# Kernel tuning notes

Hardware: AMD Instinct MI355X
Metric: run time of the kernel (lower is better)

The kernel has to match this reference:

```python
import jax, jax.numpy as jnp
import numpy as np

N = 100000          # nodes
E = 800000          # edges
H = 32              # hidden_features
L = 4               # num_layers
HS = 32             # hidden_edge_scores
EPS_BN = 1e-5
EPS_AGG = 1e-6


def _bn(x, g, b):
    # training-mode batch norm over the node/edge (batch) axis
    mu = jnp.mean(x, axis=0)
    var = jnp.var(x, axis=0)
    return (x - mu) * jax.lax.rsqrt(var + EPS_BN) * g + b


def setup_inputs() -> dict:
    key = jax.random.key(0)
    ks = jax.random.split(key, 24)
    rn = lambda k, s, sc=0.1: jax.random.normal(k, s, dtype=jnp.float32) * sc
    return {
        "x": rn(ks[0], (N, 1), 1.0),
        "e": rn(ks[1], (E, 1), 1.0),
        "edge_index": jax.random.randint(ks[2], (2, E), 0, N),
        # input projections
        "pe_w": rn(ks[3], (1, H)), "pe_b": rn(ks[4], (H,)),
        "ed_w": rn(ks[5], (1, H)), "ed_b": rn(ks[6], (H,)),
        # per-layer GatedGCN weights, stacked over layers
        "A_w": rn(ks[7], (L, H, H)), "A_b": rn(ks[8], (L, H)),
        "B_w": rn(ks[9], (L, H, H)), "B_b": rn(ks[10], (L, H)),
        "C_w": rn(ks[11], (L, H, H)), "C_b": rn(ks[12], (L, H)),
        "U_w": rn(ks[13], (L, H, H)), "U_b": rn(ks[14], (L, H)),
        "V_w": rn(ks[15], (L, H, H)), "V_b": rn(ks[16], (L, H)),
        # batch-norm affine params
        "bn_h_g": jnp.ones((L, H), jnp.float32), "bn_h_b": jnp.zeros((L, H), jnp.float32),
        "bn_e_g": jnp.ones((L, H), jnp.float32), "bn_e_b": jnp.zeros((L, H), jnp.float32),
        # score predictor: concat(src_h, dst_h, e) -> HS -> 1
        "W1_w": rn(ks[17], (3 * H, HS)), "W1_b": rn(ks[18], (HS,)),
        "W2_w": rn(ks[19], (HS, 1)), "W2_b": rn(ks[20], (1,)),
    }


def reference(x, e, edge_index, pe_w, pe_b, ed_w, ed_b,
              A_w, A_b, B_w, B_b, C_w, C_b, U_w, U_b, V_w, V_b,
              bn_h_g, bn_h_b, bn_e_g, bn_e_b, W1_w, W1_b, W2_w, W2_b):
    src, dst = edge_index[0], edge_index[1]
    h = x @ pe_w + pe_b          # [N, H]
    e = e @ ed_w + ed_b          # [E, H]
    n = h.shape[0]
    for l in range(L):
        Ah = h @ A_w[l] + A_b[l]
        Bh = h @ B_w[l] + B_b[l]
        Ce = e @ C_w[l] + C_b[l]
        Uh = h @ U_w[l] + U_b[l]
        Vh = h @ V_w[l] + V_b[l]
        # edge update: gather node features to edges
        e_new = Ah[dst] + Bh[src] + Ce               # [E, H]
        sigma = jax.nn.sigmoid(e_new)                # edge gates
        # gated mean aggregation: scatter-add to dst nodes
        num = jax.ops.segment_sum(sigma * Vh[src], dst, num_segments=n)
        den = jax.ops.segment_sum(sigma, dst, num_segments=n)
        h_new = Uh + num / (den + EPS_AGG)           # [N, H]
        # BN -> ReLU -> residual
        h = h + jax.nn.relu(_bn(h_new, bn_h_g[l], bn_h_b[l]))
        e = e + jax.nn.relu(_bn(e_new, bn_e_g[l], bn_e_b[l]))
    # score predictor over edges
    z = jnp.concatenate([h[src], h[dst], e], axis=1)  # [E, 3H]
    scores = jax.nn.relu(z @ W1_w + W1_b) @ W2_w + W2_b  # [E, 1]
    return scores
```

## Files before the change

### kernel.cpp

```cpp
#include <hip/hip_runtime.h>
#include <hip/hip_bf16.h>
#include <hip/hip_fp16.h>

#define NLAYERS 4
#define GRID_STRIDE 2048

typedef _Float16 half8_t __attribute__((ext_vector_type(8)));
typedef float float4_t __attribute__((ext_vector_type(4)));
typedef float float8_t __attribute__((ext_vector_type(8)));

__device__ __forceinline__ int permcol(int pos) { return (pos >> 1) | ((pos & 1) << 4); }

__device__ __forceinline__ void unp4(uint2 r, float* f)
{
    float2 a = __half22float2(*(__half2*)&r.x);
    float2 b = __half22float2(*(__half2*)&r.y);
    f[0] = a.x; f[1] = a.y; f[2] = b.x; f[3] = b.y;
}

__device__ __forceinline__ uint2 pk4(float f0, float f1, float f2, float f3)
{
    __half2 a = __floats2half2_rn(f0, f1), b = __floats2half2_rn(f2, f3);
    uint2 r;
    r.x = *(unsigned*)&a; r.y = *(unsigned*)&b;
    return r;
}

__global__ void zero_ints(int* __restrict__ p, int n)
{
    int i = blockIdx.x * 256 + threadIdx.x;
    if (i < n) p[i] = 0;
}

__global__ void hist_kernel(const int* __restrict__ dsts, int* __restrict__ counts, int E)
{
    int i = blockIdx.x * 256 + threadIdx.x;
    if (i < E) atomicAdd(&counts[dsts[i]], 1);
}

__global__ __launch_bounds__(256) void scan1(const int* __restrict__ counts,
                                             int* __restrict__ offsets,
                                             int* __restrict__ blocksums, int N)
{
    __shared__ int sdata[256];
    int t = threadIdx.x;
    int bbase = blockIdx.x * 1024;
    int v[4]; int s = 0;
#pragma unroll
    for (int q = 0; q < 4; q++) {
        int idx = bbase + t * 4 + q;
        v[q] = (idx < N) ? counts[idx] : 0;
        s += v[q];
    }
    sdata[t] = s;
    __syncthreads();
    for (int off = 1; off < 256; off <<= 1) {
        int x = (t >= off) ? sdata[t - off] : 0;
        __syncthreads();
        sdata[t] += x;
        __syncthreads();
    }
    int excl = sdata[t] - s;
    int run = excl;
#pragma unroll
    for (int q = 0; q < 4; q++) {
        int idx = bbase + t * 4 + q;
        if (idx < N) offsets[idx] = run;
        run += v[q];
    }
    if (t == 255) blocksums[blockIdx.x] = sdata[255];
}

__global__ void scan2(int* __restrict__ blocksums, int nb)
{
    if (threadIdx.x == 0 && blockIdx.x == 0) {
        int run = 0;
        for (int b = 0; b < nb; b++) { int t = blocksums[b]; blocksums[b] = run; run += t; }
    }
}

__global__ void scan3(int* __restrict__ offsets, const int* __restrict__ blocksums,
                      int* __restrict__ cursor, int N)
{
    int i = blockIdx.x * 256 + threadIdx.x;
    if (i < N) {
        int v = offsets[i] + blocksums[i >> 10];
        offsets[i] = v;
        cursor[i] = v;
    }
}

__global__ void scatter_perm(const int* __restrict__ dsts, int* __restrict__ cursor,
                             int* __restrict__ perm, int E, int N)
{
    int g = blockIdx.x & 7;
    int lo = (int)((long long)N * g >> 3);
    int hi = (int)((long long)N * (g + 1) >> 3);
    int nbg = gridDim.x >> 3;
    int bg = blockIdx.x >> 3;
    for (int i = bg * 256 + threadIdx.x; i < E; i += nbg * 256) {
        int d = dsts[i];
        if (d >= lo && d < hi) {
            int slot = atomicAdd(&cursor[d], 1);
            perm[slot] = i;
        }
    }
}

__global__ void gather_sd(const int* __restrict__ perm, const int* __restrict__ srcs,
                          const int* __restrict__ dsts, int* __restrict__ srcp,
                          int* __restrict__ dstp, int E)
{
    int i = blockIdx.x * 256 + threadIdx.x;
    if (i < E) {
        int e = perm[i];
        srcp[i] = srcs[e];
        dstp[i] = dsts[e];
    }
}

__global__ void init_proj4(const float* __restrict__ in, const float* __restrict__ w,
                           const float* __restrict__ b, float4* __restrict__ out, size_t n4)
{
    size_t i = (size_t)blockIdx.x * 256 + threadIdx.x;
    if (i < n4) {
        int j4 = (int)(i & 7) * 4;
        float xv = in[i >> 3];
        int c0 = permcol(j4), c1 = permcol(j4 + 1), c2 = permcol(j4 + 2), c3 = permcol(j4 + 3);
        out[i] = make_float4(fmaf(xv, w[c0], b[c0]), fmaf(xv, w[c1], b[c1]),
                             fmaf(xv, w[c2], b[c2]), fmaf(xv, w[c3], b[c3]));
    }
}

__global__ void init_ep16(const float* __restrict__ e_in, const int* __restrict__ perm,
                          const float* __restrict__ w, const float* __restrict__ b,
                          __half2* __restrict__ out, size_t n4)
{
    size_t i = (size_t)blockIdx.x * 256 + threadIdx.x;
    if (i < n4) {
        int row = (int)(i >> 3);
        float xv = e_in[perm[row]];
        int j4 = (int)(i & 7) * 4;
        int c0 = permcol(j4), c1 = permcol(j4 + 1), c2 = permcol(j4 + 2), c3 = permcol(j4 + 3);
        out[i * 2]     = __floats2half2_rn(fmaf(xv, w[c0], b[c0]), fmaf(xv, w[c1], b[c1]));
        out[i * 2 + 1] = __floats2half2_rn(fmaf(xv, w[c2], b[c2]), fmaf(xv, w[c3], b[c3]));
    }
}

template <int FUSE>
__global__ __launch_bounds__(256) void node_gemm(
    float* __restrict__ h, const float* __restrict__ hnew_in,
    const float* __restrict__ sc_h, const float* __restrict__ sh_h,
    const float* __restrict__ Aw, const float* __restrict__ Ab,
    const float* __restrict__ Bw, const float* __restrict__ Bb,
    const float* __restrict__ Uw, const float* __restrict__ Ub,
    const float* __restrict__ Vw, const float* __restrict__ Vb,
    __half* __restrict__ Ahh, __half* __restrict__ Bhh,
    float* __restrict__ Uhh, __half* __restrict__ Vhh, int N)
{
    int tid = threadIdx.x;
    int lane = tid & 63;
    int m = lane & 15, q = lane >> 4;
    half8_t bA0, bA1, bB0, bB1, bU0, bU1, bV0, bV1;
    float scq[8], shq[8];
#pragma unroll
    for (int i = 0; i < 8; i++) {
        int k = q * 8 + i;
        int kr = permcol(k);
        bA0[i] = (_Float16)Aw[kr * 32 + m];  bA1[i] = (_Float16)Aw[kr * 32 + m + 16];
        bB0[i] = (_Float16)Bw[kr * 32 + m];  bB1[i] = (_Float16)Bw[kr * 32 + m + 16];
        bU0[i] = (_Float16)Uw[kr * 32 + m];  bU1[i] = (_Float16)Uw[kr * 32 + m + 16];
        bV0[i] = (_Float16)Vw[kr * 32 + m];  bV1[i] = (_Float16)Vw[kr * 32 + m + 16];
        if (FUSE) { scq[i] = sc_h[k]; shq[i] = sh_h[k]; }
    }
    float ab0 = Ab[m], ab1 = Ab[m + 16];
    float bb0 = Bb[m], bb1 = Bb[m + 16];
    float ub0 = Ub[m], ub1 = Ub[m + 16];
    float vb0 = Vb[m], vb1 = Vb[m + 16];

    int ntile = (N + 15) >> 4;
    int wid = blockIdx.x * 4 + (tid >> 6);
    int nwave = gridDim.x * 4;
    for (int t = wid; t < ntile; t += nwave) {
        int base = t << 4;
        int arow = base + m;
        bool valid = arow < N;
        if (!valid) arow = N - 1;
        float8_t hv = *(const float8_t*)(h + (size_t)arow * 32 + q * 8);
        if (FUSE) {
            float8_t pv = *(const float8_t*)(hnew_in + (size_t)arow * 32 + q * 8);
#pragma unroll
            for (int i = 0; i < 8; i++)
                hv[i] += fmaxf(fmaf(pv[i], scq[i], shq[i]), 0.f);
            if (valid) *(float8_t*)(h + (size_t)arow * 32 + q * 8) = hv;
        }
        half8_t a;
#pragma unroll
        for (int i = 0; i < 8; i++) a[i] = (_Float16)hv[i];
        float4_t aA0 = __builtin_amdgcn_mfma_f32_16x16x32_f16(a, bA0, (float4_t){0,0,0,0}, 0, 0, 0);
        float4_t aA1 = __builtin_amdgcn_mfma_f32_16x16x32_f16(a, bA1, (float4_t){0,0,0,0}, 0, 0, 0);
        float4_t aB0 = __builtin_amdgcn_mfma_f32_16x16x32_f16(a, bB0, (float4_t){0,0,0,0}, 0, 0, 0);
        float4_t aB1 = __builtin_amdgcn_mfma_f32_16x16x32_f16(a, bB1, (float4_t){0,0,0,0}, 0, 0, 0);
        float4_t aU0 = __builtin_amdgcn_mfma_f32_16x16x32_f16(a, bU0, (float4_t){0,0,0,0}, 0, 0, 0);
        float4_t aU1 = __builtin_amdgcn_mfma_f32_16x16x32_f16(a, bU1, (float4_t){0,0,0,0}, 0, 0, 0);
        float4_t aV0 = __builtin_amdgcn_mfma_f32_16x16x32_f16(a, bV0, (float4_t){0,0,0,0}, 0, 0, 0);
        float4_t aV1 = __builtin_amdgcn_mfma_f32_16x16x32_f16(a, bV1, (float4_t){0,0,0,0}, 0, 0, 0);
#pragma unroll
        for (int reg = 0; reg < 4; reg++) {
            int node = base + q * 4 + reg;
            if (node < N) {
                size_t o = (size_t)node * 32;
                *(__half2*)(Ahh + o + 2 * m) = __floats2half2_rn(aA0[reg] + ab0, aA1[reg] + ab1);
                *(__half2*)(Bhh + o + 2 * m) = __floats2half2_rn(aB0[reg] + bb0, aB1[reg] + bb1);
                *(__half2*)(Vhh + o + 2 * m) = __floats2half2_rn(aV0[reg] + vb0, aV1[reg] + vb1);
                *(float2*)(Uhh + o + 2 * m)  = make_float2(aU0[reg] + ub0, aU1[reg] + ub1);
            }
        }
    }
}

__global__ __launch_bounds__(256) void edge_en(
    const __half* __restrict__ ep,
    const int* __restrict__ srcp, const int* __restrict__ dstp,
    const __half* __restrict__ Ah, const __half* __restrict__ Bh,
    const float* __restrict__ Cw, const float* __restrict__ Cb,
    __half* __restrict__ enh, float* __restrict__ partial, int E)
{
    __shared__ float red[256];
    int tid = threadIdx.x;
    int lane = tid & 63;
    int m = lane & 15, q = lane >> 4;
    half8_t b0, b1;
#pragma unroll
    for (int i = 0; i < 8; i++) {
        int k = q * 8 + i;
        int kr = permcol(k);
        b0[i] = (_Float16)Cw[kr * 32 + m];
        b1[i] = (_Float16)Cw[kr * 32 + m + 16];
    }
    float cb0 = Cb[m], cb1 = Cb[m + 16];
    float es0 = 0.f, eq0 = 0.f, es1 = 0.f, eq1 = 0.f;

    int ntile = (E + 15) >> 4;
    int wid = blockIdx.x * 4 + (tid >> 6);
    int nwave = gridDim.x * 4;
    for (int t = wid; t < ntile; t += nwave) {
        int base = t << 4;
        int arow = base + m;
        if (arow >= E) arow = E - 1;
        half8_t a = *(const half8_t*)(ep + (size_t)arow * 32 + q * 8);
        float4_t acc0 = __builtin_amdgcn_mfma_f32_16x16x32_f16(a, b0, (float4_t){0.f,0.f,0.f,0.f}, 0, 0, 0);
        float4_t acc1 = __builtin_amdgcn_mfma_f32_16x16x32_f16(a, b1, (float4_t){0.f,0.f,0.f,0.f}, 0, 0, 0);
#pragma unroll
        for (int reg = 0; reg < 4; reg++) {
            int row = q * 4 + reg;
            int edge = base + row;
            if (edge < E) {
                int s = srcp[edge], d = dstp[edge];
                float2 ah = __half22float2(*(const __half2*)(Ah + (size_t)d * 32 + 2 * m));
                float2 bh = __half22float2(*(const __half2*)(Bh + (size_t)s * 32 + 2 * m));
                float en0 = acc0[reg] + cb0 + ah.x + bh.x;
                float en1 = acc1[reg] + cb1 + ah.y + bh.y;
                *(__half2*)(enh + (size_t)edge * 32 + 2 * m) = __floats2half2_rn(en0, en1);
                es0 += en0; eq0 += en0 * en0;
                es1 += en1; eq1 += en1 * en1;
            }
        }
    }
    float* p = partial + (size_t)blockIdx.x * 64;
    __syncthreads();
    red[tid] = es0;
    __syncthreads();
    if (tid < 16) {
        float s = 0.f;
#pragma unroll
        for (int w = 0; w < 4; w++)
#pragma unroll
            for (int k = 0; k < 4; k++) s += red[w * 64 + k * 16 + tid];
        p[2 * tid] = s;
    }
    __syncthreads();
    red[tid] = es1;
    __syncthreads();
    if (tid < 16) {
        float s = 0.f;
#pragma unroll
        for (int w = 0; w < 4; w++)
#pragma unroll
            for (int k = 0; k < 4; k++) s += red[w * 64 + k * 16 + tid];
        p[2 * tid + 1] = s;
    }
    __syncthreads();
    red[tid] = eq0;
    __syncthreads();
    if (tid < 16) {
        float s = 0.f;
#pragma unroll
        for (int w = 0; w < 4; w++)
#pragma unroll
            for (int k = 0; k < 4; k++) s += red[w * 64 + k * 16 + tid];
        p[32 + 2 * tid] = s;
    }
    __syncthreads();
    red[tid] = eq1;
    __syncthreads();
    if (tid < 16) {
        float s = 0.f;
#pragma unroll
        for (int w = 0; w < 4; w++)
#pragma unroll
            for (int k = 0; k < 4; k++) s += red[w * 64 + k * 16 + tid];
        p[32 + 2 * tid + 1] = s;
    }
}

__global__ __launch_bounds__(256) void node_agg(
    const __half* __restrict__ enh, const int* __restrict__ srcp,
    const int* __restrict__ offsets, const int* __restrict__ counts,
    const __half* __restrict__ Vh, float* __restrict__ hnew,
    __half* __restrict__ ep, const float* __restrict__ sc_e, const float* __restrict__ sh_e,
    float* __restrict__ partial, int N)
{
    __shared__ float red[512];
    int tid = threadIdx.x, u = tid & 7, grp = tid >> 3;
    int c0 = 4 * u;
    float sc[4], sh[4];
#pragma unroll
    for (int k = 0; k < 4; k++) { sc[k] = sc_e[c0 + k]; sh[k] = sh_e[c0 + k]; }
    float hs[4] = {0.f, 0.f, 0.f, 0.f}, hq[4] = {0.f, 0.f, 0.f, 0.f};

    for (int nb0 = blockIdx.x * 32; nb0 < N; nb0 += gridDim.x * 32) {
        int node = nb0 + grp;
        if (node >= N) break;
        int start = offsets[node], len = counts[node];
        float num[4] = {0.f, 0.f, 0.f, 0.f}, den[4] = {0.f, 0.f, 0.f, 0.f};
        int qq = 0;
        for (; qq + 2 <= len; qq += 2) {
            int p0 = start + qq, p1 = p0 + 1;
            int s0 = srcp[p0], s1 = srcp[p1];
            uint2 enr0 = *(const uint2*)(enh + (size_t)p0 * 32 + c0);
            uint2 enr1 = *(const uint2*)(enh + (size_t)p1 * 32 + c0);
            uint2 vhr0 = *(const uint2*)(Vh + (size_t)s0 * 32 + c0);
            uint2 vhr1 = *(const uint2*)(Vh + (size_t)s1 * 32 + c0);
            uint2 epr0 = *(const uint2*)(ep + (size_t)p0 * 32 + c0);
            uint2 epr1 = *(const uint2*)(ep + (size_t)p1 * 32 + c0);
            float en0[4], en1[4], vh0[4], vh1[4], ev0[4], ev1[4];
            unp4(enr0, en0); unp4(enr1, en1);
            unp4(vhr0, vh0); unp4(vhr1, vh1);
            unp4(epr0, ev0); unp4(epr1, ev1);
            float o0[4], o1[4];
#pragma unroll
            for (int k = 0; k < 4; k++) {
                float sg0 = 1.f / (1.f + __expf(-en0[k]));
                float sg1 = 1.f / (1.f + __expf(-en1[k]));
                num[k] = fmaf(sg0, vh0[k], num[k]);
                num[k] = fmaf(sg1, vh1[k], num[k]);
                den[k] += sg0 + sg1;
                o0[k] = ev0[k] + fmaxf(fmaf(en0[k], sc[k], sh[k]), 0.f);
                o1[k] = ev1[k] + fmaxf(fmaf(en1[k], sc[k], sh[k]), 0.f);
            }
            *(uint2*)(ep + (size_t)p0 * 32 + c0) = pk4(o0[0], o0[1], o0[2], o0[3]);
            *(uint2*)(ep + (size_t)p1 * 32 + c0) = pk4(o1[0], o1[1], o1[2], o1[3]);
        }
        if (qq < len) {
            int p0 = start + qq;
            int s0 = srcp[p0];
            uint2 enr0 = *(const uint2*)(enh + (size_t)p0 * 32 + c0);
            uint2 vhr0 = *(const uint2*)(Vh + (size_t)s0 * 32 + c0);
            uint2 epr0 = *(const uint2*)(ep + (size_t)p0 * 32 + c0);
            float en0[4], vh0[4], ev0[4];
            unp4(enr0, en0); unp4(vhr0, vh0); unp4(epr0, ev0);
            float o0[4];
#pragma unroll
            for (int k = 0; k < 4; k++) {
                float sg0 = 1.f / (1.f + __expf(-en0[k]));
                num[k] = fmaf(sg0, vh0[k], num[k]);
                den[k] += sg0;
                o0[k] = ev0[k] + fmaxf(fmaf(en0[k], sc[k], sh[k]), 0.f);
            }
            *(uint2*)(ep + (size_t)p0 * 32 + c0) = pk4(o0[0], o0[1], o0[2], o0[3]);
        }
        size_t ho = (size_t)node * 32 + c0;
        float4 uh = *(const float4*)(hnew + ho);
        float hv[4];
        hv[0] = uh.x + num[0] / (den[0] + 1e-6f);
        hv[1] = uh.y + num[1] / (den[1] + 1e-6f);
        hv[2] = uh.z + num[2] / (den[2] + 1e-6f);
        hv[3] = uh.w + num[3] / (den[3] + 1e-6f);
        *(float4*)(hnew + ho) = make_float4(hv[0], hv[1], hv[2], hv[3]);
#pragma unroll
        for (int k = 0; k < 4; k++) { hs[k] += hv[k]; hq[k] += hv[k] * hv[k]; }
    }

    float* p = partial + (size_t)blockIdx.x * 64;
#pragma unroll
    for (int k = 0; k < 4; k++) {
        __syncthreads();
        red[tid] = hs[k]; red[256 + tid] = hq[k];
        __syncthreads();
        if (tid < 8) {
            float s = 0.f;
#pragma unroll
            for (int g = 0; g < 32; g++) s += red[g * 8 + tid];
            p[4 * tid + k] = s;
        } else if (tid < 16) {
            int uu = tid - 8;
            float s = 0.f;
#pragma unroll
            for (int g = 0; g < 32; g++) s += red[256 + g * 8 + uu];
            p[32 + 4 * uu + k] = s;
        }
    }
}

__global__ __launch_bounds__(256) void stats_side(
    const float* __restrict__ partial, int nrows, double cnt,
    const float* __restrict__ g, const float* __restrict__ b,
    float* __restrict__ sc_out, float* __restrict__ sh_out)
{
    int j = blockIdx.x;
    int col = (j >> 1) | ((j & 1) << 4);
    __shared__ double rs[256], rq[256];
    double s = 0.0, q = 0.0;
    for (int r = threadIdx.x; r < nrows; r += 256) {
        s += (double)partial[(size_t)r * 64 + j];
        q += (double)partial[(size_t)r * 64 + 32 + j];
    }
    rs[threadIdx.x] = s; rq[threadIdx.x] = q;
    __syncthreads();
    for (int off = 128; off; off >>= 1) {
        if (threadIdx.x < off) { rs[threadIdx.x] += rs[threadIdx.x + off]; rq[threadIdx.x] += rq[threadIdx.x + off]; }
        __syncthreads();
    }
    if (threadIdx.x == 0) {
        double mean = rs[0] / cnt;
        double var = rq[0] / cnt - mean * mean;
        float scale = g[col] * (float)(1.0 / sqrt(var + 1e-5));
        sc_out[j] = scale;
        sh_out[j] = b[col] - (float)mean * scale;
    }
}

__global__ void apply4_h16(const float4* __restrict__ pre, const float* __restrict__ scale,
                           const float* __restrict__ shift, const float4* __restrict__ hold,
                           __half2* __restrict__ h16, size_t n4)
{
    size_t i = (size_t)blockIdx.x * 256 + threadIdx.x;
    if (i < n4) {
        int j4 = (int)(i & 7) * 4;
        float4 sc = *(const float4*)(scale + j4);
        float4 sh = *(const float4*)(shift + j4);
        float4 p = pre[i], a = hold[i];
        a.x += fmaxf(fmaf(p.x, sc.x, sh.x), 0.f);
        a.y += fmaxf(fmaf(p.y, sc.y, sh.y), 0.f);
        a.z += fmaxf(fmaf(p.z, sc.z, sh.z), 0.f);
        a.w += fmaxf(fmaf(p.w, sc.w, sh.w), 0.f);
        h16[i * 2]     = __floats2half2_rn(a.x, a.y);
        h16[i * 2 + 1] = __floats2half2_rn(a.z, a.w);
    }
}

__global__ __launch_bounds__(256) void predictor(
    const __half* __restrict__ h16, const __half* __restrict__ e16,
    const int* __restrict__ srcp, const int* __restrict__ dstp, const int* __restrict__ perm,
    const float* __restrict__ W1, const float* __restrict__ b1,
    const float* __restrict__ W2, const float* __restrict__ b2v,
    float* __restrict__ out, int E)
{
    int tid = threadIdx.x;
    int lane = tid & 63;
    int m = lane & 15, q = lane >> 4;
    half8_t bf00, bf01, bf10, bf11, bf20, bf21;
#pragma unroll
    for (int i = 0; i < 8; i++) {
        int k = q * 8 + i;
        int kr = permcol(k);
        bf00[i] = (_Float16)W1[kr * 32 + m];
        bf01[i] = (_Float16)W1[kr * 32 + m + 16];
        bf10[i] = (_Float16)W1[(32 + kr) * 32 + m];
        bf11[i] = (_Float16)W1[(32 + kr) * 32 + m + 16];
        bf20[i] = (_Float16)W1[(64 + kr) * 32 + m];
        bf21[i] = (_Float16)W1[(64 + kr) * 32 + m + 16];
    }
    float b10 = b1[m], b11 = b1[m + 16];
    float w20 = W2[m], w21 = W2[m + 16];
    float b2 = b2v[0];

    int ntile = (E + 15) >> 4;
    int wid = blockIdx.x * 4 + (tid >> 6);
    int nwave = gridDim.x * 4;
    for (int t = wid; t < ntile; t += nwave) {
        int base = t << 4;
        int arow = base + m;
        if (arow >= E) arow = E - 1;
        int s = srcp[arow], d = dstp[arow];
        half8_t a0 = *(const half8_t*)(h16 + (size_t)s * 32 + q * 8);
        half8_t a1 = *(const half8_t*)(h16 + (size_t)d * 32 + q * 8);
        half8_t a2 = *(const half8_t*)(e16 + (size_t)arow * 32 + q * 8);
        float4_t acc0 = {0.f, 0.f, 0.f, 0.f}, acc1 = {0.f, 0.f, 0.f, 0.f};
        acc0 = __builtin_amdgcn_mfma_f32_16x16x32_f16(a0, bf00, acc0, 0, 0, 0);
        acc1 = __builtin_amdgcn_mfma_f32_16x16x32_f16(a0, bf01, acc1, 0, 0, 0);
        acc0 = __builtin_amdgcn_mfma_f32_16x16x32_f16(a1, bf10, acc0, 0, 0, 0);
        acc1 = __builtin_amdgcn_mfma_f32_16x16x32_f16(a1, bf11, acc1, 0, 0, 0);
        acc0 = __builtin_amdgcn_mfma_f32_16x16x32_f16(a2, bf20, acc0, 0, 0, 0);
        acc1 = __builtin_amdgcn_mfma_f32_16x16x32_f16(a2, bf21, acc1, 0, 0, 0);
#pragma unroll
        for (int reg = 0; reg < 4; reg++) {
            float tp = fmaxf(acc0[reg] + b10, 0.f) * w20
                     + fmaxf(acc1[reg] + b11, 0.f) * w21;
            tp += __shfl_xor(tp, 1);
            tp += __shfl_xor(tp, 2);
            tp += __shfl_xor(tp, 4);
            tp += __shfl_xor(tp, 8);
            int idx = base + q * 4 + reg;
            if (m == 0 && idx < E) {
                int oe = perm[idx];
                out[oe] = tp + b2;
            }
        }
    }
}

extern "C" void kernel_launch(void* const* d_in, const int* in_sizes, int n_in,
                              void* d_out, int out_size, void* d_ws, size_t ws_size,
                              hipStream_t stream)
{
    const int N = in_sizes[0];
    const int E = in_sizes[1];

    const float* x    = (const float*)d_in[0];
    const float* e_in = (const float*)d_in[1];
    const int*   eidx = (const int*)d_in[2];
    const float* pe_w = (const float*)d_in[3];
    const float* pe_b = (const float*)d_in[4];
    const float* ed_w = (const float*)d_in[5];
    const float* ed_b = (const float*)d_in[6];
    const float* Aw = (const float*)d_in[7];
    const float* Ab = (const float*)d_in[8];
    const float* Bw = (const float*)d_in[9];
    const float* Bb = (const float*)d_in[10];
    const float* Cw = (const float*)d_in[11];
    const float* Cb = (const float*)d_in[12];
    const float* Uw = (const float*)d_in[13];
    const float* Ub = (const float*)d_in[14];
    const float* Vw = (const float*)d_in[15];
    const float* Vb = (const float*)d_in[16];
    const float* bn_h_g = (const float*)d_in[17];
    const float* bn_h_b = (const float*)d_in[18];
    const float* bn_e_g = (const float*)d_in[19];
    const float* bn_e_b = (const float*)d_in[20];
    const float* W1w = (const float*)d_in[21];
    const float* W1b = (const float*)d_in[22];
    const float* W2w = (const float*)d_in[23];
    const float* W2b = (const float*)d_in[24];

    const int* srcs = eidx;
    const int* dsts = eidx + E;

    size_t nh = (size_t)N * 32;
    size_t eh = (size_t)E * 32;

    float* ws = (float*)d_ws;
    float* stats     = ws;
    float* partial_h = stats + 128;
    float* partial_e = partial_h + GRID_STRIDE * 64;
    float* h    = partial_e + GRID_STRIDE * 64;
    float* hnew = h + nh;
    __half* Ah  = (__half*)(hnew + nh);
    __half* Bh  = Ah + nh;
    __half* Vh  = Bh + nh;
    __half* ep  = Vh + nh;
    __half* enh = ep + eh;
    int* counts    = (int*)(enh + eh);
    int* offsets   = counts + N;
    int* cursor    = offsets + N;
    int* blocksums = cursor + N;
    int* perm      = blocksums + 128;
    int* srcp      = perm + E;
    int* dstp      = srcp + E;

    size_t nh4 = nh / 4, eh4 = eh / 4;
    int gh4 = (int)((nh4 + 255) / 256);
    int ge4 = (int)((eh4 + 255) / 256);
    int gN = (N + 255) / 256;
    int gE = (E + 255) / 256;
    int nb = (N + 1023) / 1024;
    int ntileN = (N + 15) / 16;
    int gGemm = (ntileN + 3) / 4;
    if (gGemm > GRID_STRIDE) gGemm = GRID_STRIDE;

    zero_ints<<<gN, 256, 0, stream>>>(counts, N);
    hist_kernel<<<gE, 256, 0, stream>>>(dsts, counts, E);
    scan1<<<nb, 256, 0, stream>>>(counts, offsets, blocksums, N);
    scan2<<<1, 64, 0, stream>>>(blocksums, nb);
    scan3<<<gN, 256, 0, stream>>>(offsets, blocksums, cursor, N);
    scatter_perm<<<GRID_STRIDE, 256, 0, stream>>>(dsts, cursor, perm, E, N);
    gather_sd<<<gE, 256, 0, stream>>>(perm, srcs, dsts, srcp, dstp, E);

    init_proj4<<<gh4, 256, 0, stream>>>(x, pe_w, pe_b, (float4*)h, nh4);
    init_ep16<<<ge4, 256, 0, stream>>>(e_in, perm, ed_w, ed_b, (__half2*)ep, eh4);

    for (int l = 0; l < NLAYERS; l++) {
        if (l == 0)
            node_gemm<0><<<gGemm, 256, 0, stream>>>(h, hnew, stats + 0, stats + 32,
                Aw + l * 1024, Ab + l * 32, Bw + l * 1024, Bb + l * 32,
                Uw + l * 1024, Ub + l * 32, Vw + l * 1024, Vb + l * 32,
                Ah, Bh, hnew, Vh, N);
        else
            node_gemm<1><<<gGemm, 256, 0, stream>>>(h, hnew, stats + 0, stats + 32,
                Aw + l * 1024, Ab + l * 32, Bw + l * 1024, Bb + l * 32,
                Uw + l * 1024, Ub + l * 32, Vw + l * 1024, Vb + l * 32,
                Ah, Bh, hnew, Vh, N);
        edge_en<<<GRID_STRIDE, 256, 0, stream>>>(ep, srcp, dstp, Ah, Bh,
            Cw + l * 1024, Cb + l * 32, enh, partial_e, E);
        stats_side<<<32, 256, 0, stream>>>(partial_e, GRID_STRIDE, (double)E,
            bn_e_g + l * 32, bn_e_b + l * 32, stats + 64, stats + 96);
        node_agg<<<GRID_STRIDE, 256, 0, stream>>>(enh, srcp, offsets, counts,
            Vh, hnew, ep, stats + 64, stats + 96, partial_h, N);
        stats_side<<<32, 256, 0, stream>>>(partial_h, GRID_STRIDE, (double)N,
            bn_h_g + l * 32, bn_h_b + l * 32, stats + 0, stats + 32);
    }

    apply4_h16<<<gh4, 256, 0, stream>>>((const float4*)hnew, stats + 0, stats + 32,
                                        (const float4*)h, (__half2*)Ah, nh4);

    predictor<<<GRID_STRIDE, 256, 0, stream>>>((const __half*)Ah, (const __half*)ep,
                                               srcp, dstp, perm, W1w, W1b, W2w, W2b,
                                               (float*)d_out, E);
}
```

Before: 723.3 us.

## Defer edge residual update into next layer's edge kernel and predictor

The edge BN/ReLU/residual update (e += relu(bn(e_new))) moves out of node_agg. It is now applied lazily at the start of the next layer's edge_en, and in the predictor for the last layer. This takes the ep read and write out of the node aggregation loop and avoids a separate pass over edge features. node_agg and the edge stats pass no longer depend on each other, and sigmoid and division switch to hardware reciprocal approximations. The cost is that the predictor and later edge_en calls must also read enh, and fast reciprocal slightly lowers accuracy.

```diff
diff --git a/kernel.cpp b/kernel.cpp
--- a/kernel.cpp
+++ b/kernel.cpp
@@ -18,12 +18,9 @@
     f[0] = a.x; f[1] = a.y; f[2] = b.x; f[3] = b.y;
 }
 
-__device__ __forceinline__ uint2 pk4(float f0, float f1, float f2, float f3)
-{
-    __half2 a = __floats2half2_rn(f0, f1), b = __floats2half2_rn(f2, f3);
-    uint2 r;
-    r.x = *(unsigned*)&a; r.y = *(unsigned*)&b;
-    return r;
+__device__ __forceinline__ float fast_sigmoid(float x)
+{
+    return __builtin_amdgcn_rcpf(1.f + __expf(-x));
 }
 
 __global__ void zero_ints(int* __restrict__ p, int n)
@@ -219,24 +216,28 @@
     }
 }
 
+template <int FIRST>
 __global__ __launch_bounds__(256) void edge_en(
-    const __half* __restrict__ ep,
+    __half* __restrict__ ep, __half* __restrict__ enh,
     const int* __restrict__ srcp, const int* __restrict__ dstp,
     const __half* __restrict__ Ah, const __half* __restrict__ Bh,
     const float* __restrict__ Cw, const float* __restrict__ Cb,
-    __half* __restrict__ enh, float* __restrict__ partial, int E)
+    const float* __restrict__ sc_e, const float* __restrict__ sh_e,
+    float* __restrict__ partial, int E)
 {
     __shared__ float red[256];
     int tid = threadIdx.x;
     int lane = tid & 63;
     int m = lane & 15, q = lane >> 4;
     half8_t b0, b1;
+    float sca[8], sha[8];
 #pragma unroll
     for (int i = 0; i < 8; i++) {
         int k = q * 8 + i;
         int kr = permcol(k);
         b0[i] = (_Float16)Cw[kr * 32 + m];
         b1[i] = (_Float16)Cw[kr * 32 + m + 16];
+        if (!FIRST) { sca[i] = sc_e[k]; sha[i] = sh_e[k]; }
     }
     float cb0 = Cb[m], cb1 = Cb[m + 16];
     float es0 = 0.f, eq0 = 0.f, es1 = 0.f, eq1 = 0.f;
@@ -247,8 +248,18 @@
     for (int t = wid; t < ntile; t += nwave) {
         int base = t << 4;
         int arow = base + m;
-        if (arow >= E) arow = E - 1;
-        half8_t a = *(const half8_t*)(ep + (size_t)arow * 32 + q * 8);
+        bool avalid = arow < E;
+        int ar = avalid ? arow : E - 1;
+        half8_t a = *(const half8_t*)(ep + (size_t)ar * 32 + q * 8);
+        if (!FIRST) {
+            half8_t enp = *(const half8_t*)(enh + (size_t)ar * 32 + q * 8);
+#pragma unroll
+            for (int i = 0; i < 8; i++) {
+                float ev = (float)a[i] + fmaxf(fmaf((float)enp[i], sca[i], sha[i]), 0.f);
+                a[i] = (_Float16)ev;
+            }
+            if (avalid) *(half8_t*)(ep + (size_t)ar * 32 + q * 8) = a;
+        }
         float4_t acc0 = __builtin_amdgcn_mfma_f32_16x16x32_f16(a, b0, (float4_t){0.f,0.f,0.f,0.f}, 0, 0, 0);
         float4_t acc1 = __builtin_amdgcn_mfma_f32_16x16x32_f16(a, b1, (float4_t){0.f,0.f,0.f,0.f}, 0, 0, 0);
 #pragma unroll
@@ -318,15 +329,11 @@
     const __half* __restrict__ enh, const int* __restrict__ srcp,
     const int* __restrict__ offsets, const int* __restrict__ counts,
     const __half* __restrict__ Vh, float* __restrict__ hnew,
-    __half* __restrict__ ep, const float* __restrict__ sc_e, const float* __restrict__ sh_e,
     float* __restrict__ partial, int N)
 {
     __shared__ float red[512];
     int tid = threadIdx.x, u = tid & 7, grp = tid >> 3;
     int c0 = 4 * u;
-    float sc[4], sh[4];
-#pragma unroll
-    for (int k = 0; k < 4; k++) { sc[k] = sc_e[c0 + k]; sh[k] = sh_e[c0 + k]; }
     float hs[4] = {0.f, 0.f, 0.f, 0.f}, hq[4] = {0.f, 0.f, 0.f, 0.f};
 
     for (int nb0 = blockIdx.x * 32; nb0 < N; nb0 += gridDim.x * 32) {
@@ -342,51 +349,40 @@
             uint2 enr1 = *(const uint2*)(enh + (size_t)p1 * 32 + c0);
             uint2 vhr0 = *(const uint2*)(Vh + (size_t)s0 * 32 + c0);
             uint2 vhr1 = *(const uint2*)(Vh + (size_t)s1 * 32 + c0);
-            uint2 epr0 = *(const uint2*)(ep + (size_t)p0 * 32 + c0);
-            uint2 epr1 = *(const uint2*)(ep + (size_t)p1 * 32 + c0);
-            float en0[4], en1[4], vh0[4], vh1[4], ev0[4], ev1[4];
+            float en0[4], en1[4], vh0[4], vh1[4];
             unp4(enr0, en0); unp4(enr1, en1);
             unp4(vhr0, vh0); unp4(vhr1, vh1);
-            unp4(epr0, ev0); unp4(epr1, ev1);
-            float o0[4], o1[4];
 #pragma unroll
             for (int k = 0; k < 4; k++) {
-                float sg0 = 1.f / (1.f + __expf(-en0[k]));
-                float sg1 = 1.f / (1.f + __expf(-en1[k]));
+                float sg0 = fast_sigmoid(en0[k]);
+                float sg1 = fast_sigmoid(en1[k]);
                 num[k] = fmaf(sg0, vh0[k], num[k]);
                 num[k] = fmaf(sg1, vh1[k], num[k]);
                 den[k] += sg0 + sg1;
-                o0[k] = ev0[k] + fmaxf(fmaf(en0[k], sc[k], sh[k]), 0.f);
-                o1[k] = ev1[k] + fmaxf(fmaf(en1[k], sc[k], sh[k]), 0.f);
             }
-            *(uint2*)(ep + (size_t)p0 * 32 + c0) = pk4(o0[0], o0[1], o0[2], o0[3]);
-            *(uint2*)(ep + (size_t)p1 * 32 + c0) = pk4(o1[0], o1[1], o1[2], o1[3]);
         }
         if (qq < len) {
             int p0 = start + qq;
             int s0 = srcp[p0];
             uint2 enr0 = *(const uint2*)(enh + (size_t)p0 * 32 + c0);
             uint2 vhr0 = *(const uint2*)(Vh + (size_t)s0 * 32 + c0);
-            uint2 epr0 = *(const uint2*)(ep + (size_t)p0 * 32 + c0);
-            float en0[4], vh0[4], ev0[4];
-            unp4(enr0, en0); unp4(vhr0, vh0); unp4(epr0, ev0);
-            float o0[4];
+            float en0[4], vh0[4];
+            unp4(enr0, en0); unp4(vhr0, vh0);
 #pragma unroll
             for (int k = 0; k < 4; k++) {
-                float sg0 = 1.f / (1.f + __expf(-en0[k]));
+                float sg0 = fast_sigmoid(en0[k]);
                 num[k] = fmaf(sg0, vh0[k], num[k]);
                 den[k] += sg0;
-                o0[k] = ev0[k] + fmaxf(fmaf(en0[k], sc[k], sh[k]), 0.f);
             }
-            *(uint2*)(ep + (size_t)p0 * 32 + c0) = pk4(o0[0], o0[1], o0[2], o0[3]);
         }
         size_t ho = (size_t)node * 32 + c0;
         float4 uh = *(const float4*)(hnew + ho);
         float hv[4];
-        hv[0] = uh.x + num[0] / (den[0] + 1e-6f);
-        hv[1] = uh.y + num[1] / (den[1] + 1e-6f);
-        hv[2] = uh.z + num[2] / (den[2] + 1e-6f);
-        hv[3] = uh.w + num[3] / (den[3] + 1e-6f);
+#pragma unroll
+        for (int k = 0; k < 4; k++) {
+            float* up = (float*)&uh;
+            hv[k] = up[k] + num[k] * __builtin_amdgcn_rcpf(den[k] + 1e-6f);
+        }
         *(float4*)(hnew + ho) = make_float4(hv[0], hv[1], hv[2], hv[3]);
 #pragma unroll
         for (int k = 0; k < 4; k++) { hs[k] += hv[k]; hq[k] += hv[k] * hv[k]; }
@@ -461,8 +457,10 @@
 }
 
 __global__ __launch_bounds__(256) void predictor(
-    const __half* __restrict__ h16, const __half* __restrict__ e16,
+    const __half* __restrict__ h16, const __half* __restrict__ ep,
+    const __half* __restrict__ enh,
     const int* __restrict__ srcp, const int* __restrict__ dstp, const int* __restrict__ perm,
+    const float* __restrict__ sc_e, const float* __restrict__ sh_e,
     const float* __restrict__ W1, const float* __restrict__ b1,
     const float* __restrict__ W2, const float* __restrict__ b2v,
     float* __restrict__ out, int E)
@@ -471,6 +469,7 @@
     int lane = tid & 63;
     int m = lane & 15, q = lane >> 4;
     half8_t bf00, bf01, bf10, bf11, bf20, bf21;
+    float scq[8], shq[8];
 #pragma unroll
     for (int i = 0; i < 8; i++) {
         int k = q * 8 + i;
@@ -481,6 +480,7 @@
         bf11[i] = (_Float16)W1[(32 + kr) * 32 + m + 16];
         bf20[i] = (_Float16)W1[(64 + kr) * 32 + m];
         bf21[i] = (_Float16)W1[(64 + kr) * 32 + m + 16];
+        scq[i] = sc_e[k]; shq[i] = sh_e[k];
     }
     float b10 = b1[m], b11 = b1[m + 16];
     float w20 = W2[m], w21 = W2[m + 16];
@@ -496,7 +496,14 @@
         int s = srcp[arow], d = dstp[arow];
         half8_t a0 = *(const half8_t*)(h16 + (size_t)s * 32 + q * 8);
         half8_t a1 = *(const half8_t*)(h16 + (size_t)d * 32 + q * 8);
-        half8_t a2 = *(const half8_t*)(e16 + (size_t)arow * 32 + q * 8);
+        half8_t ee = *(const half8_t*)(ep + (size_t)arow * 32 + q * 8);
+        half8_t enr = *(const half8_t*)(enh + (size_t)arow * 32 + q * 8);
+        half8_t a2;
+#pragma unroll
+        for (int i = 0; i < 8; i++) {
+            float evv = (float)ee[i] + fmaxf(fmaf((float)enr[i], scq[i], shq[i]), 0.f);
+            a2[i] = (_Float16)evv;
+        }
         float4_t acc0 = {0.f, 0.f, 0.f, 0.f}, acc1 = {0.f, 0.f, 0.f, 0.f};
         acc0 = __builtin_amdgcn_mfma_f32_16x16x32_f16(a0, bf00, acc0, 0, 0, 0);
         acc1 = __builtin_amdgcn_mfma_f32_16x16x32_f16(a0, bf01, acc1, 0, 0, 0);
@@ -611,12 +618,16 @@
                 Aw + l * 1024, Ab + l * 32, Bw + l * 1024, Bb + l * 32,
                 Uw + l * 1024, Ub + l * 32, Vw + l * 1024, Vb + l * 32,
                 Ah, Bh, hnew, Vh, N);
-        edge_en<<<GRID_STRIDE, 256, 0, stream>>>(ep, srcp, dstp, Ah, Bh,
-            Cw + l * 1024, Cb + l * 32, enh, partial_e, E);
+        if (l == 0)
+            edge_en<1><<<GRID_STRIDE, 256, 0, stream>>>(ep, enh, srcp, dstp, Ah, Bh,
+                Cw + l * 1024, Cb + l * 32, stats + 64, stats + 96, partial_e, E);
+        else
+            edge_en<0><<<GRID_STRIDE, 256, 0, stream>>>(ep, enh, srcp, dstp, Ah, Bh,
+                Cw + l * 1024, Cb + l * 32, stats + 64, stats + 96, partial_e, E);
+        node_agg<<<GRID_STRIDE, 256, 0, stream>>>(enh, srcp, offsets, counts,
+            Vh, hnew, partial_h, N);
         stats_side<<<32, 256, 0, stream>>>(partial_e, GRID_STRIDE, (double)E,
             bn_e_g + l * 32, bn_e_b + l * 32, stats + 64, stats + 96);
-        node_agg<<<GRID_STRIDE, 256, 0, stream>>>(enh, srcp, offsets, counts,
-            Vh, hnew, ep, stats + 64, stats + 96, partial_h, N);
         stats_side<<<32, 256, 0, stream>>>(partial_h, GRID_STRIDE, (double)N,
             bn_h_g + l * 32, bn_h_b + l * 32, stats + 0, stats + 32);
     }
@@ -624,7 +635,8 @@
     apply4_h16<<<gh4, 256, 0, stream>>>((const float4*)hnew, stats + 0, stats + 32,
                                         (const float4*)h, (__half2*)Ah, nh4);
 
-    predictor<<<GRID_STRIDE, 256, 0, stream>>>((const __half*)Ah, (const __half*)ep,
-                                               srcp, dstp, perm, W1w, W1b, W2w, W2b,
+    predictor<<<GRID_STRIDE, 256, 0, stream>>>((const __half*)Ah, ep, enh,
+                                               srcp, dstp, perm, stats + 64, stats + 96,
+                                               W1w, W1b, W2w, W2b,
                                                (float*)d_out, E);
 }
```

Result: no change. 723.0 us (-0.0%).
